# Optimization experiments

Measured on AMD Instinct MI355X. Metric: run time of the kernel, lower is better.

The kernel has to match this reference:

```python
import jax, jax.numpy as jnp
import numpy as np

# V:N:M sparsity config (n=2 kept of m=8 per vector-block; mask pattern [1,0,1,0,0,0,0,0])
M_BLK = 8
KEEP_OFFSETS = np.array([0, 2], dtype=np.int32)  # positions kept in each m-block
B, S, D_IN, D_OUT = 2, 8192, 4096, 4096
K_KEPT = D_IN // M_BLK * len(KEEP_OFFSETS)  # 1024


def _keep_idx():
    # column indices of the surviving weight entries (same for every output row)
    blocks = np.arange(D_IN // M_BLK, dtype=np.int32)[:, None] * M_BLK  # [D_IN/M,1]
    return jnp.asarray((blocks + KEEP_OFFSETS[None, :]).reshape(-1))   # [K_KEPT]


def setup_inputs() -> dict:
    key = jax.random.key(0)
    k1, k2, k3 = jax.random.split(key, 3)
    x = jax.random.normal(k1, (B, S, D_IN), dtype=jnp.float32)
    values = jax.random.normal(k2, (D_OUT, K_KEPT), dtype=jnp.float32) * 0.02
    bias = jax.random.normal(k3, (D_OUT,), dtype=jnp.float32) * 0.02
    return {"x": x, "values": values, "bias": bias}


def reference(x, values, bias):
    # Sparse SpMM: gather kept input features, dense GEMM with compressed values.
    # Equivalent to x @ (masked dense W).T + bias, without materializing W.
    keep = _keep_idx()               # [K_KEPT] int32, constant metadata
    xg = x[..., keep]                # [B,S,K_KEPT]
    out = jnp.einsum('bsk,nk->bsn', xg, values) + bias  # [B,S,D_OUT]
    return out
```

## Files before the change

kernel.cpp:

```cpp
#include <hip/hip_runtime.h>
#include <hip/hip_bf16.h>


#define M_TOTAL 16384
#define DIN     4096
#define KDIM    1024
#define NDIM    4096

typedef unsigned short u16;
typedef unsigned int   u32;
typedef __bf16 bf16x8 __attribute__((ext_vector_type(8)));
typedef float  f32x4  __attribute__((ext_vector_type(4)));
typedef float  f32x16 __attribute__((ext_vector_type(16)));

typedef const void __attribute__((address_space(1)))* gp_t;
typedef void __attribute__((address_space(3)))*       lp_t;

__device__ __forceinline__ u16 f2bf(float f) {
    u32 u = __float_as_uint(f);
    u += 0x7FFFu + ((u >> 16) & 1u);
    return (u16)(u >> 16);
}
__device__ __forceinline__ u32 pack2(float a, float b) {
    return (u32)f2bf(a) | ((u32)f2bf(b) << 16);
}

__global__ void prep_kernel(const float* __restrict__ x, uint2* __restrict__ xg2,
                            const float* __restrict__ vals, uint4* __restrict__ vb4) {
    const int tid = threadIdx.x;
    if (blockIdx.x < 4096) {
        int i = blockIdx.x * 256 + tid;
        const int stride = 4096 * 256;
#pragma unroll
        for (int it = 0; it < 4; ++it, i += stride) {
            const f32x4* p = (const f32x4*)(x + (size_t)i * 16);
            f32x4 f0 = __builtin_nontemporal_load(p);
            f32x4 f1 = __builtin_nontemporal_load(p + 2);
            xg2[i] = make_uint2(pack2(f0.x, f0.z), pack2(f1.x, f1.z));
        }
    } else {
        const int i = (blockIdx.x - 4096) * 256 + tid;
        const f32x4* p = (const f32x4*)(vals + (size_t)i * 8);
        f32x4 a = __builtin_nontemporal_load(p);
        f32x4 b = __builtin_nontemporal_load(p + 1);
        vb4[i] = make_uint4(pack2(a.x, a.y), pack2(a.z, a.w),
                            pack2(b.x, b.y), pack2(b.z, b.w));
    }
}


#define LDSA(d, kh) (((d) * 2 + (kh)) * 16384)
#define LDSB(d, kh) (65536 + ((d) * 2 + (kh)) * 16384)

#define LOADA(d, kh, mh) { _Pragma("unroll") \
    for (int mm = 0; mm < 2; ++mm) { _Pragma("unroll") \
    for (int ks = 0; ks < 2; ++ks) \
        af[mm * 2 + ks] = *(const bf16x8*)(lds + LDSA(d, kh) \
            + (wr * 8 + ((mh) * 2 + mm) * 2) * 1024 + fl_base \
            + (((ks << 5) + acol) ^ aswz)); } }

#define LOADB(d, kh) { _Pragma("unroll") \
    for (int nn = 0; nn < 2; ++nn) { _Pragma("unroll") \
    for (int ks = 0; ks < 2; ++ks) \
        bfr[nn * 2 + ks] = *(const bf16x8*)(lds + LDSB(d, kh) \
            + (wc * 4 + nn * 2) * 1024 + fl_base \
            + (((ks << 5) + acol) ^ aswz)); } }

#define MFMA8(mh) { \
    __builtin_amdgcn_s_setprio(1); \
    _Pragma("unroll") for (int mm = 0; mm < 2; ++mm) \
    _Pragma("unroll") for (int nn = 0; nn < 2; ++nn) \
    _Pragma("unroll") for (int ks = 0; ks < 2; ++ks) \
        acc[(mh) * 2 + mm][nn] = __builtin_amdgcn_mfma_f32_32x32x16_bf16( \
            af[mm * 2 + ks], bfr[nn * 2 + ks], acc[(mh) * 2 + mm][nn], 0, 0, 0); \
    __builtin_amdgcn_s_setprio(0); }

#define BAR() __builtin_amdgcn_s_barrier()
#define VMCNT6() asm volatile("s_waitcnt vmcnt(6)" ::: "memory")

__global__ __launch_bounds__(512, 2) void gemm_kernel(
    const u16* __restrict__ A, const u16* __restrict__ Bv,
    const float* __restrict__ bias, float* __restrict__ C)
{
    __shared__ __align__(1024) char lds[131072];

    const int tid  = threadIdx.x;
    const int lane = tid & 63;
    const int wid  = tid >> 6;
    const int wr   = wid >> 2;
    const int wc   = wid & 3;

    const int bb   = blockIdx.x;
    const int btm0 = (bb & 7) * 8 + (bb >> 7);
    const int btn  = (bb >> 3) & 15;

    const int st_r0 = wid * 16 + (lane >> 2);
    const int st_ck = ((lane & 3) * 8) ^ ((tid & 32) >> 1) ^ ((tid & 64) >> 3);
    const u16* A0  = A  + (size_t)(btm0 * 256 + st_r0) * KDIM + st_ck;
    const u16* Bs0 = Bv + (size_t)(btn  * 256 + st_r0) * KDIM + st_ck;
    const int dst0 = tid * 16;

    const int fl_base = (lane & 15) * 64 + ((lane >> 4) & 1) * 1024;
    const int aswz    = (((lane >> 3) & 1) << 5) ^ (((lane >> 4) & 1) << 4);
    const int acol    = ((lane >> 5) & 1) * 16;

    auto STAGE = [&](const u16* as_, int s) {
        const int kt = s >> 2, j = s & 3;
        const int d = kt & 1, kh = (j >> 1) & 1;
        const int ko = kt * 64 + kh * 32;
        const u16* src = (j & 1) ? Bs0 : as_;
        const int base = ((j & 1) ? 65536 : 0) + (d * 2 + kh) * 16384;
        __builtin_amdgcn_global_load_lds((gp_t)(src + ko),
            (lp_t)(lds + base + dst0), 16, 0, 0);
        __builtin_amdgcn_global_load_lds((gp_t)(src + 128 * KDIM + ko),
            (lp_t)(lds + base + 8192 + dst0), 16, 0, 0);
    };

    const int c_colb = btn * 256 + wc * 64 + (lane & 31);
    float bvr[2];
#pragma unroll
    for (int n = 0; n < 2; ++n) bvr[n] = bias[c_colb + n * 32];

    f32x16 acc[4][2] = {};
    bf16x8 af[4], bfr[4];

    STAGE(A0, 0); STAGE(A0, 1); STAGE(A0, 2); STAGE(A0, 3);
    STAGE(A0, 4); STAGE(A0, 5); STAGE(A0, 6);
    VMCNT6();
    BAR();

#pragma unroll 1
    for (int r = 0; r < 4; ++r) {
        const u16* Ar = A0 + (size_t)r * 512 * KDIM;
        const u16* An = (r < 3) ? (Ar + 512 * KDIM) : Ar;

#pragma unroll 1
        for (int t = 0; t < 7; ++t) {
            const int s0 = 8 * t + 7;
            LOADB(0, 0); LOADA(0, 0, 0); STAGE(Ar, s0);     BAR(); MFMA8(0); BAR();
            LOADA(0, 0, 1);              STAGE(Ar, s0 + 1); BAR(); MFMA8(1); BAR();
            LOADB(0, 1); LOADA(0, 1, 0); STAGE(Ar, s0 + 2); BAR(); MFMA8(0); BAR();
            LOADA(0, 1, 1);              STAGE(Ar, s0 + 3); BAR(); MFMA8(1);
            VMCNT6(); BAR();
            LOADB(1, 0); LOADA(1, 0, 0); STAGE(Ar, s0 + 4); BAR(); MFMA8(0); BAR();
            LOADA(1, 0, 1);              STAGE(Ar, s0 + 5); BAR(); MFMA8(1); BAR();
            LOADB(1, 1); LOADA(1, 1, 0); STAGE(Ar, s0 + 6); BAR(); MFMA8(0); BAR();
            LOADA(1, 1, 1);              STAGE(Ar, s0 + 7); BAR(); MFMA8(1);
            VMCNT6(); BAR();
        }
        LOADB(0, 0); LOADA(0, 0, 0); STAGE(Ar, 63); BAR(); MFMA8(0); BAR();
        LOADA(0, 0, 1);              STAGE(An, 0);  BAR(); MFMA8(1); BAR();
        LOADB(0, 1); LOADA(0, 1, 0); STAGE(An, 1);  BAR(); MFMA8(0); BAR();
        LOADA(0, 1, 1);              STAGE(An, 2);  BAR(); MFMA8(1);
        VMCNT6(); BAR();
        LOADB(1, 0); LOADA(1, 0, 0); STAGE(An, 3);  BAR(); MFMA8(0); BAR();
        LOADA(1, 0, 1);              STAGE(An, 4);  BAR(); MFMA8(1); BAR();
        LOADB(1, 1); LOADA(1, 1, 0); STAGE(An, 5);  BAR(); MFMA8(0); BAR();
        LOADA(1, 1, 1);              STAGE(An, 6);  BAR(); MFMA8(1);
        VMCNT6(); BAR();

        const int c_row0 = (btm0 + 2 * r) * 256 + wr * 128 + ((lane >> 5) & 1) * 4;
#pragma unroll
        for (int mi = 0; mi < 4; ++mi) {
#pragma unroll
            for (int n = 0; n < 2; ++n) {
                f32x16 a = acc[mi][n];
#pragma unroll
                for (int q = 0; q < 4; ++q) {
#pragma unroll
                    for (int rr = 0; rr < 4; ++rr) {
                        const int row = c_row0 + mi * 32 + q * 8 + rr;
                        __builtin_nontemporal_store(a[q * 4 + rr] + bvr[n],
                            &C[(size_t)row * NDIM + c_colb + n * 32]);
                    }
                }
#pragma unroll
                for (int z = 0; z < 16; ++z) acc[mi][n][z] = 0.f;
            }
        }
    }
}

extern "C" void kernel_launch(void* const* d_in, const int* in_sizes, int n_in,
                              void* d_out, int out_size, void* d_ws, size_t ws_size,
                              hipStream_t stream) {
    const float* x      = (const float*)d_in[0];
    const float* values = (const float*)d_in[1];
    const float* bias   = (const float*)d_in[2];
    float* out = (float*)d_out;

    u16* xg = (u16*)d_ws;
    u16* vb = (u16*)((char*)d_ws + ((size_t)32 << 20));

    prep_kernel<<<6144, 256, 0, stream>>>(x, (uint2*)xg, values, (uint4*)vb);
    gemm_kernel<<<256, 512, 0, stream>>>(xg, vb, bias, out);
}
```

Before: 205.7 us.

## Use 4 waves with 128x128 warp tiles and restructured staging pipeline

Shrinks the GEMM block from 8 to 4 waves, with each wave computing a 128x128 output tile (4x4 MFMA 32x32 fragments) instead of 128x64. This raises register-level reuse of A and B fragments per LDS read and cuts the number of barriers per k-step. The LDS staging schedule becomes a per-half-k-tile phase macro with vmcnt waits, and output stores drop the nontemporal hint. In exchange it uses many more VGPRs/AGPRs per wave and leaves fewer waves to hide latency.

```diff
diff --git a/kernel.cpp b/kernel.cpp
--- a/kernel.cpp
+++ b/kernel.cpp
@@ -49,36 +49,34 @@
 }
 
 
-#define LDSA(d, kh) (((d) * 2 + (kh)) * 16384)
-#define LDSB(d, kh) (65536 + ((d) * 2 + (kh)) * 16384)
-
-#define LOADA(d, kh, mh) { _Pragma("unroll") \
-    for (int mm = 0; mm < 2; ++mm) { _Pragma("unroll") \
+#define LOADA(d, kh) { _Pragma("unroll") \
+    for (int mf = 0; mf < 4; ++mf) { _Pragma("unroll") \
     for (int ks = 0; ks < 2; ++ks) \
-        af[mm * 2 + ks] = *(const bf16x8*)(lds + LDSA(d, kh) \
-            + (wr * 8 + ((mh) * 2 + mm) * 2) * 1024 + fl_base \
-            + (((ks << 5) + acol) ^ aswz)); } }
+        af[mf * 2 + ks] = *(const bf16x8*)(lds + ((d) * 2 + (kh)) * 16384 \
+            + (wr2 * 8 + 2 * mf) * 1024 + fl_base + (((ks << 5) + acol) ^ aswz)); } }
 
 #define LOADB(d, kh) { _Pragma("unroll") \
-    for (int nn = 0; nn < 2; ++nn) { _Pragma("unroll") \
+    for (int nf = 0; nf < 4; ++nf) { _Pragma("unroll") \
     for (int ks = 0; ks < 2; ++ks) \
-        bfr[nn * 2 + ks] = *(const bf16x8*)(lds + LDSB(d, kh) \
-            + (wc * 4 + nn * 2) * 1024 + fl_base \
-            + (((ks << 5) + acol) ^ aswz)); } }
+        bfr[nf * 2 + ks] = *(const bf16x8*)(lds + 65536 + ((d) * 2 + (kh)) * 16384 \
+            + (wc2 * 8 + 2 * nf) * 1024 + fl_base + (((ks << 5) + acol) ^ aswz)); } }
 
-#define MFMA8(mh) { \
+#define MFMA32() { \
     __builtin_amdgcn_s_setprio(1); \
-    _Pragma("unroll") for (int mm = 0; mm < 2; ++mm) \
-    _Pragma("unroll") for (int nn = 0; nn < 2; ++nn) \
     _Pragma("unroll") for (int ks = 0; ks < 2; ++ks) \
-        acc[(mh) * 2 + mm][nn] = __builtin_amdgcn_mfma_f32_32x32x16_bf16( \
-            af[mm * 2 + ks], bfr[nn * 2 + ks], acc[(mh) * 2 + mm][nn], 0, 0, 0); \
+    _Pragma("unroll") for (int mf = 0; mf < 4; ++mf) \
+    _Pragma("unroll") for (int nf = 0; nf < 4; ++nf) \
+        acc[mf][nf] = __builtin_amdgcn_mfma_f32_32x32x16_bf16( \
+            af[mf * 2 + ks], bfr[nf * 2 + ks], acc[mf][nf], 0, 0, 0); \
     __builtin_amdgcn_s_setprio(0); }
 
-#define BAR() __builtin_amdgcn_s_barrier()
-#define VMCNT6() asm volatile("s_waitcnt vmcnt(6)" ::: "memory")
+#define BAR()  __builtin_amdgcn_s_barrier()
+#define VM16() asm volatile("s_waitcnt vmcnt(16)" ::: "memory")
+#define VM63() asm volatile("s_waitcnt vmcnt(63)" ::: "memory")
 
-__global__ __launch_bounds__(512, 2) void gemm_kernel(
+#define PH(W, d, kh, STG) { W; BAR(); LOADA(d, kh); LOADB(d, kh); STG; BAR(); MFMA32(); }
+
+__global__ __launch_bounds__(256, 1) void gemm_kernel(
     const u16* __restrict__ A, const u16* __restrict__ Bv,
     const float* __restrict__ bias, float* __restrict__ C)
 {
@@ -87,15 +85,15 @@
     const int tid  = threadIdx.x;
     const int lane = tid & 63;
     const int wid  = tid >> 6;
-    const int wr   = wid >> 2;
-    const int wc   = wid & 3;
+    const int wr2  = wid >> 1;
+    const int wc2  = wid & 1;
 
     const int bb   = blockIdx.x;
     const int btm0 = (bb & 7) * 8 + (bb >> 7);
     const int btn  = (bb >> 3) & 15;
 
-    const int st_r0 = wid * 16 + (lane >> 2);
-    const int st_ck = ((lane & 3) * 8) ^ ((tid & 32) >> 1) ^ ((tid & 64) >> 3);
+    const int st_r0 = tid >> 2;
+    const int st_ck = ((tid & 3) * 8) ^ ((tid & 32) >> 1) ^ ((tid & 64) >> 3);
     const u16* A0  = A  + (size_t)(btm0 * 256 + st_r0) * KDIM + st_ck;
     const u16* Bs0 = Bv + (size_t)(btn  * 256 + st_r0) * KDIM + st_ck;
     const int dst0 = tid * 16;
@@ -104,78 +102,74 @@
     const int aswz    = (((lane >> 3) & 1) << 5) ^ (((lane >> 4) & 1) << 4);
     const int acol    = ((lane >> 5) & 1) * 16;
 
-    auto STAGE = [&](const u16* as_, int s) {
-        const int kt = s >> 2, j = s & 3;
-        const int d = kt & 1, kh = (j >> 1) & 1;
-        const int ko = kt * 64 + kh * 32;
-        const u16* src = (j & 1) ? Bs0 : as_;
-        const int base = ((j & 1) ? 65536 : 0) + (d * 2 + kh) * 16384;
-        __builtin_amdgcn_global_load_lds((gp_t)(src + ko),
-            (lp_t)(lds + base + dst0), 16, 0, 0);
-        __builtin_amdgcn_global_load_lds((gp_t)(src + 128 * KDIM + ko),
-            (lp_t)(lds + base + 8192 + dst0), 16, 0, 0);
+    auto STAGE = [&](const u16* asrc, int tt, int kh) {
+        const int d  = tt & 1;
+        const int ko = (tt & 15) * 64 + kh * 32;
+        const int ab = (d * 2 + kh) * 16384;
+#pragma unroll
+        for (int j = 0; j < 4; ++j)
+            __builtin_amdgcn_global_load_lds((gp_t)(asrc + (size_t)(64 * j) * KDIM + ko),
+                (lp_t)(lds + ab + j * 4096 + dst0), 16, 0, 0);
+#pragma unroll
+        for (int j = 0; j < 4; ++j)
+            __builtin_amdgcn_global_load_lds((gp_t)(Bs0 + (size_t)(64 * j) * KDIM + ko),
+                (lp_t)(lds + 65536 + ab + j * 4096 + dst0), 16, 0, 0);
     };
 
-    const int c_colb = btn * 256 + wc * 64 + (lane & 31);
-    float bvr[2];
+    const int c_colb = btn * 256 + wc2 * 128 + (lane & 31);
+    float bvr[4];
 #pragma unroll
-    for (int n = 0; n < 2; ++n) bvr[n] = bias[c_colb + n * 32];
+    for (int n = 0; n < 4; ++n) bvr[n] = bias[c_colb + n * 32];
 
-    f32x16 acc[4][2] = {};
-    bf16x8 af[4], bfr[4];
+    f32x16 acc[4][4] = {};
+    bf16x8 af[8], bfr[8];
 
-    STAGE(A0, 0); STAGE(A0, 1); STAGE(A0, 2); STAGE(A0, 3);
-    STAGE(A0, 4); STAGE(A0, 5); STAGE(A0, 6);
-    VMCNT6();
-    BAR();
+    STAGE(A0, 0, 0); STAGE(A0, 0, 1); STAGE(A0, 1, 0);
 
 #pragma unroll 1
     for (int r = 0; r < 4; ++r) {
         const u16* Ar = A0 + (size_t)r * 512 * KDIM;
         const u16* An = (r < 3) ? (Ar + 512 * KDIM) : Ar;
 
+        if (r == 0) {
+            PH(VM16(), 0, 0, STAGE(Ar, 1, 1));
+            PH(VM16(), 0, 1, STAGE(Ar, 2, 0));
+            PH(VM16(), 1, 0, STAGE(Ar, 2, 1));
+            PH(VM16(), 1, 1, STAGE(Ar, 3, 0));
+        } else {
+            PH(VM63(), 0, 0, STAGE(Ar, 1, 1));
+            PH(VM63(), 0, 1, STAGE(Ar, 2, 0));
+            PH(VM63(), 1, 0, STAGE(Ar, 2, 1));
+            PH(VM16(), 1, 1, STAGE(Ar, 3, 0));
+        }
+
 #pragma unroll 1
-        for (int t = 0; t < 7; ++t) {
-            const int s0 = 8 * t + 7;
-            LOADB(0, 0); LOADA(0, 0, 0); STAGE(Ar, s0);     BAR(); MFMA8(0); BAR();
-            LOADA(0, 0, 1);              STAGE(Ar, s0 + 1); BAR(); MFMA8(1); BAR();
-            LOADB(0, 1); LOADA(0, 1, 0); STAGE(Ar, s0 + 2); BAR(); MFMA8(0); BAR();
-            LOADA(0, 1, 1);              STAGE(Ar, s0 + 3); BAR(); MFMA8(1);
-            VMCNT6(); BAR();
-            LOADB(1, 0); LOADA(1, 0, 0); STAGE(Ar, s0 + 4); BAR(); MFMA8(0); BAR();
-            LOADA(1, 0, 1);              STAGE(Ar, s0 + 5); BAR(); MFMA8(1); BAR();
-            LOADB(1, 1); LOADA(1, 1, 0); STAGE(Ar, s0 + 6); BAR(); MFMA8(0); BAR();
-            LOADA(1, 1, 1);              STAGE(Ar, s0 + 7); BAR(); MFMA8(1);
-            VMCNT6(); BAR();
+        for (int tt = 2; tt < 16; tt += 2) {
+            const u16* s1 = Ar;
+            const u16* s2 = (tt + 2 < 16) ? Ar : An;
+            const u16* s3 = (tt + 3 < 16) ? Ar : An;
+            PH(VM16(), 0, 0, STAGE(s1, tt + 1, 1));
+            PH(VM16(), 0, 1, STAGE(s2, tt + 2, 0));
+            PH(VM16(), 1, 0, STAGE(s2, tt + 2, 1));
+            PH(VM16(), 1, 1, STAGE(s3, tt + 3, 0));
         }
-        LOADB(0, 0); LOADA(0, 0, 0); STAGE(Ar, 63); BAR(); MFMA8(0); BAR();
-        LOADA(0, 0, 1);              STAGE(An, 0);  BAR(); MFMA8(1); BAR();
-        LOADB(0, 1); LOADA(0, 1, 0); STAGE(An, 1);  BAR(); MFMA8(0); BAR();
-        LOADA(0, 1, 1);              STAGE(An, 2);  BAR(); MFMA8(1);
-        VMCNT6(); BAR();
-        LOADB(1, 0); LOADA(1, 0, 0); STAGE(An, 3);  BAR(); MFMA8(0); BAR();
-        LOADA(1, 0, 1);              STAGE(An, 4);  BAR(); MFMA8(1); BAR();
-        LOADB(1, 1); LOADA(1, 1, 0); STAGE(An, 5);  BAR(); MFMA8(0); BAR();
-        LOADA(1, 1, 1);              STAGE(An, 6);  BAR(); MFMA8(1);
-        VMCNT6(); BAR();
 
-        const int c_row0 = (btm0 + 2 * r) * 256 + wr * 128 + ((lane >> 5) & 1) * 4;
+        const int c_row0 = (btm0 + 2 * r) * 256 + wr2 * 128 + ((lane >> 5) & 1) * 4;
 #pragma unroll
-        for (int mi = 0; mi < 4; ++mi) {
+        for (int mf = 0; mf < 4; ++mf) {
 #pragma unroll
-            for (int n = 0; n < 2; ++n) {
-                f32x16 a = acc[mi][n];
+            for (int nf = 0; nf < 4; ++nf) {
+                f32x16 a = acc[mf][nf];
 #pragma unroll
                 for (int q = 0; q < 4; ++q) {
 #pragma unroll
                     for (int rr = 0; rr < 4; ++rr) {
-                        const int row = c_row0 + mi * 32 + q * 8 + rr;
-                        __builtin_nontemporal_store(a[q * 4 + rr] + bvr[n],
-                            &C[(size_t)row * NDIM + c_colb + n * 32]);
+                        const int row = c_row0 + mf * 32 + q * 8 + rr;
+                        C[(size_t)row * NDIM + c_colb + nf * 32] = a[q * 4 + rr] + bvr[nf];
                     }
                 }
 #pragma unroll
-                for (int z = 0; z < 16; ++z) acc[mi][n][z] = 0.f;
+                for (int z = 0; z < 16; ++z) acc[mf][nf][z] = 0.f;
             }
         }
     }
@@ -193,5 +187,5 @@
     u16* vb = (u16*)((char*)d_ws + ((size_t)32 << 20));
 
     prep_kernel<<<6144, 256, 0, stream>>>(x, (uint2*)xg, values, (uint4*)vb);
-    gemm_kernel<<<256, 512, 0, stream>>>(xg, vb, bias, out);
+    gemm_kernel<<<256, 256, 0, stream>>>(xg, vb, bias, out);
 }
```

Result: slower. 232.1 us (+12.8%).
